# Performance work log

Hardware: AMD Instinct MI355X
Metric: run time of the kernel (lower is better)

The kernel has to match this reference:

```python
import jax, jax.numpy as jnp
import numpy as np
from jax.scipy.special import xlogy

LAMBDA_XM = 0.05
LAMBDA_SEG2D = 1.0
BN_EPS = 1e-5


def setup_inputs() -> dict:
    key = jax.random.key(0)
    ks = jax.random.split(key, 40)
    S, N, Nv, B, Np, M, H, C, MID = 2, 240000, 80000, 2, 120000, 30000, 64, 20, 16
    Nimg = B * M
    f = lambda i, shape, s=0.05: jax.random.normal(ks[i], shape, jnp.float32) * s
    inp = {
        'img_feat': f(0, (S, Nimg, H), 1.0),
        'pts_feat': f(1, (S, Nv, H), 1.0),
        'coors_inv': jax.random.randint(ks[2], (S, N), 0, Nv),
        'labels': jax.random.randint(ks[3], (N,), 0, C),
        'img_label': jax.random.randint(ks[4], (Nimg,), 0, C),
        'p2img_idx': jax.random.randint(ks[5], (B, M), 0, Np),
        # multihead 3d classifiers (per scale): Linear(H,128)-ReLU-Linear(128,C)
        'w3a': f(6, (S, H, 128)), 'b3a': jnp.zeros((S, 128)),
        'w3b': f(7, (S, 128, C)), 'b3b': jnp.zeros((S, C)),
        # multihead fuse classifiers
        'wfa': f(8, (S, H, 128)), 'bfa': jnp.zeros((S, 128)),
        'wfb': f(9, (S, 128, C)), 'bfb': jnp.zeros((S, C)),
        # attention: fc1(H->H//4), fc2(H->H//4), fc3(H//2->2), conv1/conv2 (1x1 -> linear) + BN
        'fc1w': f(10, (S, H, MID)), 'fc1b': jnp.zeros((S, MID)),
        'fc2w': f(11, (S, H, MID)), 'fc2b': jnp.zeros((S, MID)),
        'fc3w': f(12, (S, 2 * MID, 2)), 'fc3b': jnp.zeros((S, 2)),
        'c1w': f(13, (S, H, H)), 'c1b': jnp.zeros((S, H)),
        'bn1g': jnp.ones((S, H)), 'bn1b': jnp.zeros((S, H)),
        'c2w': f(14, (S, H, H)), 'c2b': jnp.zeros((S, H)),
        'bn2g': jnp.ones((S, H)), 'bn2b': jnp.zeros((S, H)),
        # final classifier Linear(S*H,128)-ReLU-Linear(128,C)
        'clw1': f(15, (S * H, 128)), 'clb1': jnp.zeros((128,)),
        'clw2': f(16, (128, C)), 'clb2': jnp.zeros((C,)),
    }
    return inp


def _mlp2(x, w1, b1, w2, b2):
    return jax.nn.relu(x @ w1 + b1) @ w2 + b2


def _ce(logits, lab):
    logp = jax.nn.log_softmax(logits, -1)
    return -jnp.take_along_axis(logp, lab[:, None], axis=1).mean()


def _lovasz(probs, lab):
    # lovasz-softmax over all classes, averaged over present classes
    C = probs.shape[1]
    fg = jax.nn.one_hot(lab, C, dtype=probs.dtype)  # [N,C]
    errors = jnp.abs(fg - probs)

    def per_class(err_c, fg_c):
        order = jnp.argsort(-err_c)
        e = err_c[order]
        f = fg_c[order]
        gts = f.sum()
        inter = gts - jnp.cumsum(f)
        union = gts + jnp.cumsum(1.0 - f)
        jac = 1.0 - inter / union
        jac = jnp.concatenate([jac[:1], jac[1:] - jac[:-1]])
        return jnp.dot(e, jac)

    losses = jax.vmap(per_class)(errors.T, fg.T)  # [C]
    present = (fg.sum(0) > 0).astype(probs.dtype)
    return jnp.sum(losses * present) / jnp.maximum(present.sum(), 1.0)


def _seg_loss(logits, lab):
    return _ce(logits, lab) + _lovasz(jax.nn.softmax(logits, -1), lab)


def _convbn_relu(x, cw, cb, g, b):
    # 1x1 Conv1d == per-point linear; BN (training-mode batch stats over points)
    y = x @ cw + cb
    mu = y.mean(0)
    var = y.var(0)
    return jax.nn.relu((y - mu) * jax.lax.rsqrt(var + BN_EPS) * g + b)


def reference(img_feat, pts_feat, coors_inv, labels, img_label, p2img_idx,
              w3a, b3a, w3b, b3b, wfa, bfa, wfb, bfb,
              fc1w, fc1b, fc2w, fc2b, fc3w, fc3b,
              c1w, c1b, bn1g, bn1b, c2w, c2b, bn2g, bn2b,
              clw1, clb1, clw2, clb2):
    S, Nv, H = pts_feat.shape
    C = w3b.shape[-1]
    B, M = p2img_idx.shape
    N = labels.shape[0]
    Np = N // B
    # p2img_mapping: per-batch gather composed to one global gather (batch blocks are contiguous/equal)
    gidx = (jnp.arange(B)[:, None] * Np + p2img_idx).reshape(-1)  # [Nimg]

    loss = jnp.float32(0.0)
    feats = []
    for s in range(S):
        pred3d = _mlp2(pts_feat[s], w3a[s], b3a[s], w3b[s], b3b[s])  # [Nv,C]
        # voxelize_labels: majority vote per voxel (== unique+scatter_max count argmax)
        counts = jnp.zeros((Nv, C), jnp.float32).at[coors_inv[s], labels].add(1.0)
        vox_lab = jnp.argmax(counts, axis=1)  # [Nv]
        # gather voxel feats/preds to image-projected points (fused gather)
        idx = coors_inv[s][gidx]  # [Nimg]
        p = pts_feat[s][idx]      # [Nimg,H] pseudo feats
        pts_pred = pred3d[idx]    # [Nimg,C]
        v = img_feat[s]           # [Nimg,H] valid (image) feats
        # Attention fusion
        w = jax.nn.sigmoid(
            jnp.concatenate([p @ fc1w[s] + fc1b[s], v @ fc2w[s] + fc2b[s]], -1) @ fc3w[s] + fc3b[s])  # [Nimg,2]
        fuse = (_convbn_relu(p, c1w[s], c1b[s], bn1g[s], bn1b[s]) * w[:, 0:1]
                + _convbn_relu(v, c2w[s], c2b[s], bn2g[s], bn2b[s]) * w[:, 1:2])
        feats.append(fuse)
        fuse_pred = _mlp2(fuse, wfa[s], bfa[s], wfb[s], bfb[s])
        loss = loss + _seg_loss(pred3d, vox_lab)
        loss = loss + _seg_loss(fuse_pred, img_label) * LAMBDA_SEG2D / S
        # F.kl_div(log_softmax(pts_pred), softmax(fuse_pred)), reduction='mean' over all elements
        pf = jax.nn.softmax(fuse_pred, -1)
        kl = jnp.mean(xlogy(pf, pf) - pf * jax.nn.log_softmax(pts_pred, -1))
        loss = loss + kl * LAMBDA_XM / S
    img_logits = _mlp2(jnp.concatenate(feats, -1), clw1, clb1, clw2, clb2)
    loss = loss + _seg_loss(img_logits, img_label)
    return loss
```

## Files before the change

kernel.cpp:

```cpp
#include <hip/hip_runtime.h>
#include <stdint.h>

static constexpr int NV   = 80000;
static constexpr int NPT  = 240000;
static constexpr int NIMG = 60000;
static constexpr int Hh   = 64;
static constexpr int Cc   = 20;
static constexpr int NPp  = 120000;
static constexpr int Mm   = 30000;
static constexpr int NB     = 8192;
static constexpr int NCH    = 16;
static constexpr int NBLK_GA  = (NIMG + 63) / 64;
static constexpr int NBLK_MLP = NV / 64;
static constexpr int NBLK_CNT = (NPT + 255) / 256;
static constexpr int NBLK_FILL_NV = (NV + 255) / 256;
static constexpr int NBLK_HIST = Cc * NCH;
static constexpr int NBLK_IDX  = (NIMG + 255) / 256;
#define BN_EPS 1e-5f

using bf16x8 = __attribute__((ext_vector_type(8))) short;
using f32x4  = __attribute__((ext_vector_type(4))) float;

__device__ __forceinline__ float waveReduce(float v) {
  #pragma unroll
  for (int o = 32; o > 0; o >>= 1) v += __shfl_down(v, o);
  return v;
}
__device__ __forceinline__ short f2bf(float f) {
  uint32_t u = __float_as_uint(f);
  return (short)((u + 0x7FFFu + ((u >> 16) & 1u)) >> 16);
}
__device__ __forceinline__ float bf2f(uint32_t h) { return __uint_as_float(h << 16); }
__device__ __forceinline__ uint32_t pk2(float a, float b) {
  return ((uint32_t)(uint16_t)f2bf(a)) | ((uint32_t)(uint16_t)f2bf(b) << 16);
}

struct PackDesc { const float* src; short* dst; int K, Nr, nt; };
struct PackArgs { PackDesc d[14]; };

__global__ void __launch_bounds__(256)
k_pack_zero(PackArgs pa,
            const float* __restrict__ fc1w, const float* __restrict__ fc1b,
            const float* __restrict__ fc2w, const float* __restrict__ fc2b,
            const float* __restrict__ fc3w, const float* __restrict__ fc3b,
            float* __restrict__ attEffs,
            uint4* __restrict__ zb, int zq,
            const int* __restrict__ ci0, const int* __restrict__ ci1,
            const int* __restrict__ p2img,
            int* __restrict__ idx0, int* __restrict__ idx1) {
  int bid = blockIdx.x;
  if (bid >= 384) {
    bid -= 384;
    if (bid < NBLK_IDX) {
      int i = bid * 256 + threadIdx.x;
      if (i < NIMG) idx0[i] = ci0[(i >= Mm ? NPp : 0) + p2img[i]];
    } else {
      int i = (bid - NBLK_IDX) * 256 + threadIdx.x;
      if (i < NIMG) idx1[i] = ci1[(i >= Mm ? NPp : 0) + p2img[i]];
    }
    return;
  }
  if (bid >= 128) {
    const uint4 z = make_uint4(0u, 0u, 0u, 0u);
    int i = (bid - 128) * 256 + threadIdx.x;
    for (; i < zq; i += 256 * 256) zb[i] = z;
    return;
  }
  const int stride = 128 * 256;
  for (int di = 0; di < 14; di++) {
    const float* src = pa.d[di].src;
    short* dst = pa.d[di].dst;
    int K = pa.d[di].K, Nr = pa.d[di].Nr, ntiles = pa.d[di].nt;
    int total = (K / 32) * ntiles * 512;
    for (int idx = bid * 256 + threadIdx.x; idx < total; idx += stride) {
      int j = idx & 7, lane = (idx >> 3) & 63, tile = idx >> 9;
      int nt = tile % ntiles, kt = tile / ntiles;
      int k = kt * 32 + (lane >> 4) * 8 + j;
      int n = nt * 16 + (lane & 15);
      float v = (n < Nr) ? src[(size_t)k * Nr + n] : 0.f;
      dst[idx] = f2bf(v);
    }
  }
  if (bid < 2 && threadIdx.x < 64) {
    int s = bid, t = threadIdx.x;
    const float* f1w = fc1w + s * 64 * 16; const float* f1b = fc1b + s * 16;
    const float* f2w = fc2w + s * 64 * 16; const float* f2b = fc2b + s * 16;
    const float* f3w = fc3w + s * 64;      const float* f3b = fc3b + s * 2;
    float* aE = attEffs + s * 320;
    float p0 = 0.f, p1 = 0.f, v0 = 0.f, v1 = 0.f;
    #pragma unroll
    for (int j = 0; j < 16; j++) {
      p0 = fmaf(f1w[t * 16 + j], f3w[j * 2], p0);
      p1 = fmaf(f1w[t * 16 + j], f3w[j * 2 + 1], p1);
      v0 = fmaf(f2w[t * 16 + j], f3w[(16 + j) * 2], v0);
      v1 = fmaf(f2w[t * 16 + j], f3w[(16 + j) * 2 + 1], v1);
    }
    aE[t * 2] = p0; aE[t * 2 + 1] = p1;
    aE[128 + t * 2] = v0; aE[128 + t * 2 + 1] = v1;
    if (t == 0) {
      float b0 = f3b[0], b1 = f3b[1];
      for (int j = 0; j < 16; j++) {
        b0 += f1b[j] * f3w[j * 2] + f2b[j] * f3w[(16 + j) * 2];
        b1 += f1b[j] * f3w[j * 2 + 1] + f2b[j] * f3w[(16 + j) * 2 + 1];
      }
      aE[256] = b0; aE[257] = b1;
    }
  }
}

__device__ void scanbin_body(const unsigned long long* __restrict__ H64,
                             int n, int call, float* __restrict__ lossesC5,
                             int* __restrict__ gts5, int cls) {
  __shared__ int sWC[4], sWF[4];
  __shared__ float sRedF[4];
  int t = threadIdx.x;
  int lane = t & 63, w = t >> 6;
  const uint4* Hv = (const uint4*)(H64 + (size_t)cls * NB + (size_t)t * 32);
  int locC = 0, locF = 0;
  #pragma unroll
  for (int i = 0; i < 16; i++) {
    uint4 u = Hv[i];
    locF += (int)(u.x + u.z);
    locC += (int)(u.y + u.w);
  }
  int sc = locC, sf = locF;
  #pragma unroll
  for (int o = 1; o < 64; o <<= 1) {
    int a = __shfl_up(sc, o);
    int b = __shfl_up(sf, o);
    if (lane >= o) { sc += a; sf += b; }
  }
  if (lane == 63) { sWC[w] = sc; sWF[w] = sf; }
  __syncthreads();
  int offC = 0, offF = 0, Ftot = 0;
  #pragma unroll
  for (int ww = 0; ww < 4; ww++) {
    int fc = sWF[ww];
    Ftot += fc;
    if (ww < w) { offC += sWC[ww]; offF += fc; }
  }
  int runC = offC + sc - locC;
  int runF = offF + sf - locF;
  float gts = (float)Ftot;
  float contrib = 0.f;
  #pragma unroll
  for (int i = 0; i < 16; i++) {
    uint4 u = Hv[i];
    #pragma unroll
    for (int j = 0; j < 2; j++) {
      int cnt = (int)(j ? u.w : u.y), fgc = (int)(j ? u.z : u.x);
      runC += cnt; runF += fgc;
      if (cnt > 0 && Ftot > 0) {
        float r0 = (float)(n - runC);
        float F0 = (float)(Ftot - runF);
        float r1 = r0 + (float)cnt;
        float F1 = F0 + (float)fgc;
        float emean = __uint_as_float((uint32_t)(t * 32 + i * 2 + j) << 17);
        contrib += emean * (r1 / (gts + r1 - F1) - r0 / (gts + r0 - F0));
      }
    }
  }
  contrib = waveReduce(contrib);
  if (lane == 0) sRedF[w] = contrib;
  __syncthreads();
  if (t == 0) {
    lossesC5[call * 32 + cls] = (Ftot > 0) ? (sRedF[0] + sRedF[1] + sRedF[2] + sRedF[3]) : 0.f;
    gts5[call * 32 + cls] = Ftot;
  }
}

__device__ void tile_loss(const float* __restrict__ sL, int r0, int rows, int n,
                          const int* __restrict__ lab, uint16_t* __restrict__ E,
                          float ceScale, float* __restrict__ lossAcc,
                          const float* __restrict__ pred3d, const int* __restrict__ idxg,
                          float klScale) {
  int t = threadIdx.x;
  if (t < 64) {
    float total = 0.f;
    int gr = r0 + t;
    if (gr < rows) {
      const float* l = sL + t * 21;
      float m = l[0];
      #pragma unroll
      for (int c = 1; c < Cc; c++) m = fmaxf(m, l[c]);
      float ex[Cc]; float se = 0.f;
      #pragma unroll
      for (int c = 0; c < Cc; c++) { ex[c] = expf(l[c] - m); se += ex[c]; }
      float inv = 1.f / se;
      float lse = logf(se);
      int lb = lab[gr];
      total = -(l[lb] - m - lse) * ceScale;
      #pragma unroll
      for (int c = 0; c < Cc; c++) {
        float prob = ex[c] * inv;
        int fg = (c == lb) ? 1 : 0;
        float err = fg ? (1.f - prob) : prob;
        err = fmaxf(err, 0.f);
        uint32_t key = __float_as_uint(err) >> 17;
        E[(size_t)c * n + gr] = (uint16_t)((key << 1) | (uint32_t)fg);
      }
      if (pred3d) {
        const float* q = pred3d + (size_t)idxg[gr] * Cc;
        float mq = q[0];
        #pragma unroll
        for (int c = 1; c < Cc; c++) mq = fmaxf(mq, q[c]);
        float sq = 0.f;
        #pragma unroll
        for (int c = 0; c < Cc; c++) sq += expf(q[c] - mq);
        float lsq = logf(sq);
        float kl = 0.f;
        #pragma unroll
        for (int c = 0; c < Cc; c++) {
          float lf = l[c] - m - lse;
          float pf = ex[c] * inv;
          float lq = q[c] - mq - lsq;
          kl += pf * (lf - lq);
        }
        total += kl * klScale;
      }
    }
    total = waveReduce(total);
    if (t == 0) atomicAdd(lossAcc, total);
  }
}

template<int D, bool TO_LDS>
__device__ __forceinline__ void mfma_mlp_core(const short* sXb, short* sH, float* sL,
    int r0, int rows,
    const short* __restrict__ pw1, const float* __restrict__ B1,
    const short* __restrict__ pw2, const float* __restrict__ B2,
    float* __restrict__ Out) {
  constexpr int LDB = D + 8;
  constexpr int KT1 = D / 32;
  const int t = threadIdx.x;
  const int lane = t & 63, w = t >> 6;
  const int m = lane & 15, quad = lane >> 4;
  const int rowA = 16 * w + m;
  bf16x8 a1[KT1];
  #pragma unroll
  for (int kt = 0; kt < KT1; kt++)
    a1[kt] = *(const bf16x8*)(sXb + rowA * LDB + kt * 32 + quad * 8);
  const bf16x8* b1 = (const bf16x8*)pw1;
  #pragma unroll
  for (int nt = 0; nt < 8; nt++) {
    f32x4 c = {0.f, 0.f, 0.f, 0.f};
    #pragma unroll
    for (int kt = 0; kt < KT1; kt++)
      c = __builtin_amdgcn_mfma_f32_16x16x32_bf16(a1[kt], b1[(kt * 8 + nt) * 64 + lane], c, 0, 0, 0);
    int col = nt * 16 + m;
    float bc = B1[col];
    #pragma unroll
    for (int reg = 0; reg < 4; reg++)
      sH[(16 * w + quad * 4 + reg) * 136 + col] = f2bf(fmaxf(c[reg] + bc, 0.f));
  }
  __syncthreads();
  bf16x8 a2[4];
  #pragma unroll
  for (int kt = 0; kt < 4; kt++)
    a2[kt] = *(const bf16x8*)(sH + rowA * 136 + kt * 32 + quad * 8);
  const bf16x8* b2 = (const bf16x8*)pw2;
  #pragma unroll
  for (int nt = 0; nt < 2; nt++) {
    f32x4 c = {0.f, 0.f, 0.f, 0.f};
    #pragma unroll
    for (int kt = 0; kt < 4; kt++)
      c = __builtin_amdgcn_mfma_f32_16x16x32_bf16(a2[kt], b2[(kt * 2 + nt) * 64 + lane], c, 0, 0, 0);
    int col = nt * 16 + m;
    if (col < Cc) {
      float bc = B2[col];
      #pragma unroll
      for (int reg = 0; reg < 4; reg++) {
        int rr = 16 * w + quad * 4 + reg;
        if (TO_LDS) {
          sL[rr * 21 + col] = c[reg] + bc;
        } else {
          int gr = r0 + rr;
          if (gr < rows) Out[(size_t)gr * Cc + col] = c[reg] + bc;
        }
      }
    }
  }
}

__device__ void mlp64_body(int bid0, const float* __restrict__ X,
    const short* __restrict__ pw1, const float* __restrict__ B1,
    const short* __restrict__ pw2, const float* __restrict__ B2,
    float* __restrict__ Out, int rows, char* smem) {
  short* sXb = (short*)smem;
  short* sH  = (short*)(smem + 9216);
  int t = threadIdx.x, r0 = bid0 * 64;
  for (int i = t; i < 1024; i += 256) {
    int r = i >> 4, k4 = (i & 15) * 4;
    int gr = r0 + r;
    float4 v = (gr < rows) ? *(const float4*)(X + (size_t)gr * 64 + k4)
                           : make_float4(0.f, 0.f, 0.f, 0.f);
    uint2 p; p.x = pk2(v.x, v.y); p.y = pk2(v.z, v.w);
    *(uint2*)(sXb + r * 72 + k4) = p;
  }
  __syncthreads();
  mfma_mlp_core<64, false>(sXb, sH, nullptr, r0, rows, pw1, B1, pw2, B2, Out);
}

__device__ void mlp128_loss_body(int bid0, const uint16_t* __restrict__ Xh,
    const short* __restrict__ pw1, const float* __restrict__ B1,
    const short* __restrict__ pw2, const float* __restrict__ B2,
    const int* __restrict__ lab, uint16_t* __restrict__ E, float ce,
    float* __restrict__ lossAcc, char* smem) {
  short* sXb = (short*)smem;
  short* sH  = (short*)(smem + 17408);
  int t = threadIdx.x, r0 = bid0 * 64;
  for (int i = t; i < 2048; i += 256) {
    int r = i >> 5, k4 = (i & 31) * 4;
    int gr = r0 + r;
    uint2 p = (gr < NIMG) ? *(const uint2*)(Xh + (size_t)gr * 128 + k4) : make_uint2(0u, 0u);
    *(uint2*)(sXb + r * 136 + k4) = p;
  }
  __syncthreads();
  mfma_mlp_core<128, true>(sXb, sH, (float*)sXb, r0, NIMG, pw1, B1, pw2, B2, nullptr);
  __syncthreads();
  tile_loss((float*)sXb, r0, NIMG, NIMG, lab, E, ce, lossAcc, nullptr, nullptr, 0.f);
}

__device__ void cnt_body(int bid0, const int* __restrict__ ci, const int* __restrict__ labels,
                         int* __restrict__ counts) {
  int i = bid0 * 256 + threadIdx.x;
  if (i < NPT) atomicAdd(&counts[(size_t)ci[i] * Cc + labels[i]], 1);
}

__device__ void colred_body(int bid0, const float* __restrict__ partials,
                            float* __restrict__ red64) {
  int t = threadIdx.x, j = bid0;
  float v = 0.f;
  for (int b = j; b < NBLK_GA; b += 64) v += partials[(size_t)b * 256 + t];
  red64[j * 256 + t] = v;
}

__device__ void fill_body(int bid0, const float* __restrict__ logits,
                          const int* __restrict__ vcnt,
                          int n, uint16_t* __restrict__ E,
                          float ceScale, float* __restrict__ lossAcc) {
  int i = bid0 * 256 + threadIdx.x;
  float total = 0.f;
  if (i < n) {
    const int* crow = vcnt + (size_t)i * Cc;
    int best = crow[0], lb = 0;
    #pragma unroll
    for (int k = 1; k < Cc; k++) {
      int ck = crow[k];
      if (ck > best) { best = ck; lb = k; }
    }
    const float* l = logits + (size_t)i * Cc;
    float m = l[0];
    #pragma unroll
    for (int c = 1; c < Cc; c++) m = fmaxf(m, l[c]);
    float ex[Cc]; float se = 0.f;
    #pragma unroll
    for (int c = 0; c < Cc; c++) { ex[c] = expf(l[c] - m); se += ex[c]; }
    float inv = 1.f / se;
    float lse = logf(se);
    total = -(l[lb] - m - lse) * ceScale;
    #pragma unroll
    for (int c = 0; c < Cc; c++) {
      float prob = ex[c] * inv;
      int fg = (c == lb) ? 1 : 0;
      float err = fg ? (1.f - prob) : prob;
      err = fmaxf(err, 0.f);
      uint32_t key = __float_as_uint(err) >> 17;
      E[(size_t)c * n + i] = (uint16_t)((key << 1) | (uint32_t)fg);
    }
  }
  total = waveReduce(total);
  __shared__ float sh[4];
  int lane = threadIdx.x & 63, w = threadIdx.x >> 6;
  if (lane == 0) sh[w] = total;
  __syncthreads();
  if (threadIdx.x == 0) atomicAdd(lossAcc, sh[0] + sh[1] + sh[2] + sh[3]);
}

__device__ void hist_body(int bid0, const uint16_t* __restrict__ E, int n,
                          unsigned long long* __restrict__ H64, char* smem) {
  uint32_t* lcf = (uint32_t*)smem;
  int t = threadIdx.x;
  int cls = bid0 / NCH, ch = bid0 - cls * NCH;
  int CHsz = (n + NCH - 1) / NCH;
  int i0 = ch * CHsz;
  int i1 = min(n, i0 + CHsz);
  for (int b = t; b < NB; b += 256) lcf[b] = 0u;
  __syncthreads();
  const uint16_t* Ec = E + (size_t)cls * n;
  for (int i = i0 + t; i < i1; i += 256) {
    uint32_t p = Ec[i];
    atomicAdd(&lcf[p >> 1], 0x10000u | (p & 1u));
  }
  __syncthreads();
  unsigned long long* Hc = H64 + (size_t)cls * NB;
  for (int b = t; b < NB; b += 256) {
    uint32_t v = lcf[b];
    if (v)
      atomicAdd(&Hc[b], ((unsigned long long)(v >> 16) << 32) | (v & 0xFFFFu));
  }
}

__device__ void gatt_body(int bid0, const float* __restrict__ pts, const int* __restrict__ idx,
                          const float* __restrict__ img,
                          const short* __restrict__ pc1, const float* __restrict__ c1b,
                          const short* __restrict__ pc2, const float* __restrict__ c2b,
                          const float* __restrict__ attEff,
                          uint16_t* __restrict__ y1, uint16_t* __restrict__ y2,
                          float* __restrict__ attw, float* __restrict__ partials,
                          char* smem) {
  short* sP = (short*)smem;
  short* sV = (short*)(smem + 9216);
  float* sAtt  = (float*)(smem + 18432);
  float* sStat = (float*)(smem + 20480);
  int t = threadIdx.x;
  int r0 = bid0 * 64;
  for (int i = t; i < 1024; i += 256) {
    int r = i >> 4, q = i & 15;
    int gr = r0 + r;
    float4 vp = make_float4(0.f, 0.f, 0.f, 0.f), vv = vp;
    if (gr < NIMG) {
      vp = *(const float4*)(pts + (size_t)idx[gr] * 64 + q * 4);
      vv = *(const float4*)(img + (size_t)gr * 64 + q * 4);
    }
    uint2 pp, qv;
    pp.x = pk2(vp.x, vp.y); pp.y = pk2(vp.z, vp.w);
    qv.x = pk2(vv.x, vv.y); qv.y = pk2(vv.z, vv.w);
    *(uint2*)(sP + r * 72 + q * 4) = pp;
    *(uint2*)(sV + r * 72 + q * 4) = qv;
  }
  __syncthreads();
  {
    int r = t & 63, qq = t >> 6;
    const float* aP = attEff;
    const float* aV = attEff + 128;
    float l0 = 0.f, l1 = 0.f;
    for (int k = qq * 16; k < qq * 16 + 16; k += 4) {
      uint2 up = *(const uint2*)(sP + r * 72 + k);
      uint2 uv = *(const uint2*)(sV + r * 72 + k);
      float p0 = bf2f(up.x & 0xffff), p1 = bf2f(up.x >> 16);
      float p2 = bf2f(up.y & 0xffff), p3 = bf2f(up.y >> 16);
      float v0 = bf2f(uv.x & 0xffff), v1 = bf2f(uv.x >> 16);
      float v2 = bf2f(uv.y & 0xffff), v3 = bf2f(uv.y >> 16);
      float4 wa = *(const float4*)(aP + 2 * k);
      float4 wb = *(const float4*)(aP + 2 * k + 4);
      l0 += p0 * wa.x + p1 * wa.z + p2 * wb.x + p3 * wb.z;
      l1 += p0 * wa.y + p1 * wa.w + p2 * wb.y + p3 * wb.w;
      float4 ua = *(const float4*)(aV + 2 * k);
      float4 ub = *(const float4*)(aV + 2 * k + 4);
      l0 += v0 * ua.x + v1 * ua.z + v2 * ub.x + v3 * ub.z;
      l1 += v0 * ua.y + v1 * ua.w + v2 * ub.y + v3 * ub.w;
    }
    sAtt[r * 8 + qq * 2] = l0;
    sAtt[r * 8 + qq * 2 + 1] = l1;
  }
  const int lane = t & 63, w = t >> 6;
  const int m = lane & 15, quad = lane >> 4;
  const int rowA = 16 * w + m;
  bf16x8 ap[2], av[2];
  #pragma unroll
  for (int kt = 0; kt < 2; kt++) {
    ap[kt] = *(const bf16x8*)(sP + rowA * 72 + kt * 32 + quad * 8);
    av[kt] = *(const bf16x8*)(sV + rowA * 72 + kt * 32 + quad * 8);
  }
  const bf16x8* b1 = (const bf16x8*)pc1;
  const bf16x8* b2 = (const bf16x8*)pc2;
  #pragma unroll
  for (int nt = 0; nt < 4; nt++) {
    int col = nt * 16 + m;
    f32x4 c1 = {0.f, 0.f, 0.f, 0.f}, c2 = {0.f, 0.f, 0.f, 0.f};
    #pragma unroll
    for (int kt = 0; kt < 2; kt++) {
      c1 = __builtin_amdgcn_mfma_f32_16x16x32_bf16(ap[kt], b1[(kt * 4 + nt) * 64 + lane], c1, 0, 0, 0);
      c2 = __builtin_amdgcn_mfma_f32_16x16x32_bf16(av[kt], b2[(kt * 4 + nt) * 64 + lane], c2, 0, 0, 0);
    }
    float bb1 = c1b[col], bb2 = c2b[col];
    float s1 = 0.f, q1 = 0.f, s2 = 0.f, q2 = 0.f;
    #pragma unroll
    for (int reg = 0; reg < 4; reg++) {
      int gr = r0 + 16 * w + quad * 4 + reg;
      if (gr < NIMG) {
        float v1 = c1[reg] + bb1, v2 = c2[reg] + bb2;
        y1[(size_t)gr * 64 + col] = (uint16_t)f2bf(v1);
        y2[(size_t)gr * 64 + col] = (uint16_t)f2bf(v2);
        s1 += v1; q1 = fmaf(v1, v1, q1);
        s2 += v2; q2 = fmaf(v2, v2, q2);
      }
    }
    s1 += __shfl_down(s1, 32); s1 += __shfl_down(s1, 16);
    q1 += __shfl_down(q1, 32); q1 += __shfl_down(q1, 16);
    s2 += __shfl_down(s2, 32); s2 += __shfl_down(s2, 16);
    q2 += __shfl_down(q2, 32); q2 += __shfl_down(q2, 16);
    if (lane < 16) {
      float* base = sStat + (w * 4 + nt) * 64 + lane;
      base[0]  = s1;
      base[16] = q1;
      base[32] = s2;
      base[48] = q2;
    }
  }
  __syncthreads();
  {
    int kind = t >> 6, col = t & 63;
    int nt = col >> 4, mm = col & 15;
    float v = 0.f;
    #pragma unroll
    for (int ww = 0; ww < 4; ww++)
      v += sStat[(ww * 4 + nt) * 64 + kind * 16 + mm];
    partials[(size_t)bid0 * 256 + kind * 64 + col] = v;
  }
  if (t < 64) {
    int gr = r0 + t;
    if (gr < NIMG) {
      float l0 = attEff[256] + sAtt[t * 8] + sAtt[t * 8 + 2] + sAtt[t * 8 + 4] + sAtt[t * 8 + 6];
      float l1 = attEff[257] + sAtt[t * 8 + 1] + sAtt[t * 8 + 3] + sAtt[t * 8 + 5] + sAtt[t * 8 + 7];
      attw[gr * 2]     = 1.f / (1.f + expf(-l0));
      attw[gr * 2 + 1] = 1.f / (1.f + expf(-l1));
    }
  }
}

__device__ void fusemlp_body(int bid0,
    const uint16_t* __restrict__ y1, const uint16_t* __restrict__ y2,
    const float* __restrict__ attw, const float* __restrict__ red64,
    const float* __restrict__ g1, const float* __restrict__ be1,
    const float* __restrict__ g2, const float* __restrict__ be2,
    uint16_t* __restrict__ feats, int s64,
    const short* __restrict__ pw1, const float* __restrict__ B1,
    const short* __restrict__ pw2, const float* __restrict__ B2,
    const int* __restrict__ lab, uint16_t* __restrict__ E, float ce,
    const float* __restrict__ pred3d, const int* __restrict__ idxg, float klScale,
    float* __restrict__ lossAcc, char* smem) {
  short* sXb = (short*)smem;
  short* sH  = (short*)(smem + 9216);
  float* sBn = (float*)(smem + 9216 + 17408);
  int t = threadIdx.x, r0 = bid0 * 64;
  float acc = 0.f;
  #pragma unroll 8
  for (int b = 0; b < 64; b++) acc += red64[b * 256 + t];
  float* sSum = (float*)sH;
  sSum[t] = acc;
  __syncthreads();
  if (t < 64) {
    float nn = (float)NIMG;
    float mu1 = sSum[t] / nn;
    float var1 = sSum[64 + t] / nn - mu1 * mu1;
    float a1 = g1[t] / sqrtf(var1 + BN_EPS);
    sBn[t] = a1; sBn[64 + t] = be1[t] - mu1 * a1;
    float mu2 = sSum[128 + t] / nn;
    float var2 = sSum[192 + t] / nn - mu2 * mu2;
    float a2 = g2[t] / sqrtf(var2 + BN_EPS);
    sBn[128 + t] = a2; sBn[192 + t] = be2[t] - mu2 * a2;
  }
  __syncthreads();
  for (int i = t; i < 1024; i += 256) {
    int r = i >> 4, q = i & 15;
    int gr = r0 + r;
    uint2 zp = make_uint2(0u, 0u);
    if (gr < NIMG) {
      float4 a1 = *(const float4*)(sBn + q * 4);
      float4 c1 = *(const float4*)(sBn + 64 + q * 4);
      float4 a2 = *(const float4*)(sBn + 128 + q * 4);
      float4 c2 = *(const float4*)(sBn + 192 + q * 4);
      uint2 u1 = *(const uint2*)(y1 + (size_t)gr * 64 + q * 4);
      uint2 u2 = *(const uint2*)(y2 + (size_t)gr * 64 + q * 4);
      float w0 = attw[gr * 2], w1 = attw[gr * 2 + 1];
      float zx = fmaxf(fmaf(bf2f(u1.x & 0xffff), a1.x, c1.x), 0.f) * w0
               + fmaxf(fmaf(bf2f(u2.x & 0xffff), a2.x, c2.x), 0.f) * w1;
      float zy = fmaxf(fmaf(bf2f(u1.x >> 16),   a1.y, c1.y), 0.f) * w0
               + fmaxf(fmaf(bf2f(u2.x >> 16),   a2.y, c2.y), 0.f) * w1;
      float zz = fmaxf(fmaf(bf2f(u1.y & 0xffff), a1.z, c1.z), 0.f) * w0
               + fmaxf(fmaf(bf2f(u2.y & 0xffff), a2.z, c2.z), 0.f) * w1;
      float zw = fmaxf(fmaf(bf2f(u1.y >> 16),   a1.w, c1.w), 0.f) * w0
               + fmaxf(fmaf(bf2f(u2.y >> 16),   a2.w, c2.w), 0.f) * w1;
      zp.x = pk2(zx, zy); zp.y = pk2(zz, zw);
      *(uint2*)(feats + (size_t)gr * 128 + s64 + q * 4) = zp;
    }
    *(uint2*)(sXb + r * 72 + q * 4) = zp;
  }
  __syncthreads();
  mfma_mlp_core<64, true>(sXb, sH, (float*)sXb, r0, NIMG, pw1, B1, pw2, B2, nullptr);
  __syncthreads();
  tile_loss((float*)sXb, r0, NIMG, NIMG, lab, E, ce, lossAcc, pred3d, idxg, klScale);
}

__global__ void __launch_bounds__(256)
k_mega2(const float* __restrict__ pf0, const float* __restrict__ pf1,
        const int* __restrict__ idx0, const int* __restrict__ idx1,
        const float* __restrict__ if0, const float* __restrict__ if1,
        const short* pc1w0, const short* pc1w1, const short* pc2w0, const short* pc2w1,
        const float* c1b, const float* c2b, const float* attEffs,
        uint16_t* y1a, uint16_t* y2a, uint16_t* y1b, uint16_t* y2b,
        float* attw0, float* attw1, float* partials0, float* partials1,
        const short* pw3a0, const float* b3a, const short* pw3b0, const float* b3b,
        const short* pw3a1, const short* pw3b1,
        float* pred3d0, float* pred3d1,
        const int* __restrict__ ci0, const int* __restrict__ ci1,
        const int* __restrict__ labels,
        int* __restrict__ counts0, int* __restrict__ counts1) {
  __shared__ char smem[26624];
  int bid = blockIdx.x;
  if (bid < NBLK_GA) {
    gatt_body(bid, pf0, idx0, if0, pc1w0, c1b, pc2w0, c2b, attEffs,
              y1a, y2a, attw0, partials0, smem);
    return;
  }
  bid -= NBLK_GA;
  if (bid < NBLK_GA) {
    gatt_body(bid, pf1, idx1, if1, pc1w1, c1b + 64, pc2w1, c2b + 64, attEffs + 320,
              y1b, y2b, attw1, partials1, smem);
    return;
  }
  bid -= NBLK_GA;
  if (bid < NBLK_MLP) { mlp64_body(bid, pf0, pw3a0, b3a, pw3b0, b3b, pred3d0, NV, smem); return; }
  bid -= NBLK_MLP;
  if (bid < NBLK_MLP) { mlp64_body(bid, pf1, pw3a1, b3a + 128, pw3b1, b3b + Cc, pred3d1, NV, smem); return; }
  bid -= NBLK_MLP;
  if (bid < NBLK_CNT) { cnt_body(bid, ci0, labels, counts0); return; }
  cnt_body(bid - NBLK_CNT, ci1, labels, counts1);
}

__global__ void __launch_bounds__(256)
k_fill_colred(const float* __restrict__ l0, const int* __restrict__ vc0, uint16_t* __restrict__ E0,
              const float* __restrict__ l1, const int* __restrict__ vc1, uint16_t* __restrict__ E1,
              float ce, float* __restrict__ lossAcc,
              const float* partials0, float* red64_0,
              const float* partials1, float* red64_1) {
  int bid = blockIdx.x;
  if (bid < NBLK_FILL_NV) {
    fill_body(bid, l0, vc0, NV, E0, ce, lossAcc);
    return;
  }
  bid -= NBLK_FILL_NV;
  if (bid < NBLK_FILL_NV) {
    fill_body(bid, l1, vc1, NV, E1, ce, lossAcc);
    return;
  }
  bid -= NBLK_FILL_NV;
  if (bid < 64) { colred_body(bid, partials0, red64_0); return; }
  colred_body(bid - 64, partials1, red64_1);
}

__global__ void __launch_bounds__(256)
k_fuse2_hist2(const uint16_t* y1a, const uint16_t* y2a, const float* attw0, const float* red64_0,
              const uint16_t* y1b, const uint16_t* y2b, const float* attw1, const float* red64_1,
              const float* bn1g, const float* bn1b, const float* bn2g, const float* bn2b,
              uint16_t* feats,
              const short* pwfa0, const float* bfa, const short* pwfb0, const float* bfb,
              const short* pwfa1, const short* pwfb1,
              const int* __restrict__ img_label, float ce, float kl, float* lossAcc,
              const float* pred3d0, const int* idx0, uint16_t* E3,
              const float* pred3d1, const int* idx1, uint16_t* E4,
              const uint16_t* __restrict__ E0, unsigned long long* H0,
              const uint16_t* __restrict__ E1, unsigned long long* H2) {
  __shared__ char smem[32768];
  int bid = blockIdx.x;
  if (bid < NBLK_GA) {
    fusemlp_body(bid, y1a, y2a, attw0, red64_0, bn1g, bn1b, bn2g, bn2b, feats, 0,
                 pwfa0, bfa, pwfb0, bfb,
                 img_label, E3, ce, pred3d0, idx0, kl, lossAcc, smem);
    return;
  }
  bid -= NBLK_GA;
  if (bid < NBLK_GA) {
    fusemlp_body(bid, y1b, y2b, attw1, red64_1, bn1g + 64, bn1b + 64, bn2g + 64, bn2b + 64,
                 feats, 64, pwfa1, bfa + 128, pwfb1, bfb + Cc,
                 img_label, E4, ce, pred3d1, idx1, kl, lossAcc, smem);
    return;
  }
  bid -= NBLK_GA;
  if (bid < NBLK_HIST) { hist_body(bid, E0, NV, H0, smem); return; }
  hist_body(bid - NBLK_HIST, E1, NV, H2, smem);
}

__global__ void __launch_bounds__(256)
k_finx2(const uint16_t* __restrict__ feats,
        const short* pcl1, const float* clb1, const short* pcl2, const float* clb2,
        const int* __restrict__ img_label, uint16_t* E2, float ce, float* lossAcc,
        const uint16_t* __restrict__ E3, unsigned long long* H1,
        const uint16_t* __restrict__ E4, unsigned long long* H3,
        const unsigned long long* H0, const unsigned long long* H2,
        float* lossesC5, int* gts5) {
  __shared__ char smem[34816];
  int bid = blockIdx.x;
  if (bid < NBLK_GA) {
    mlp128_loss_body(bid, feats, pcl1, clb1, pcl2, clb2, img_label, E2, ce, lossAcc, smem);
    return;
  }
  bid -= NBLK_GA;
  if (bid < NBLK_HIST) { hist_body(bid, E3, NIMG, H1, smem); return; }
  bid -= NBLK_HIST;
  if (bid < NBLK_HIST) { hist_body(bid, E4, NIMG, H3, smem); return; }
  bid -= NBLK_HIST;
  if (bid < Cc) { scanbin_body(H0, NV, 0, lossesC5, gts5, bid); return; }
  scanbin_body(H2, NV, 2, lossesC5, gts5, bid - Cc);
}

__global__ void __launch_bounds__(256)
k_hist_scan2(const uint16_t* __restrict__ E2, unsigned long long* H4,
             const unsigned long long* H1, const unsigned long long* H3,
             float* lossesC5, int* gts5) {
  __shared__ char smem[32768];
  int bid = blockIdx.x;
  if (bid < NBLK_HIST) { hist_body(bid, E2, NIMG, H4, smem); return; }
  bid -= NBLK_HIST;
  if (bid < Cc) { scanbin_body(H1, NIMG, 1, lossesC5, gts5, bid); return; }
  scanbin_body(H3, NIMG, 3, lossesC5, gts5, bid - Cc);
}

__global__ void __launch_bounds__(256)
k_scanbin5(const unsigned long long* H64, int n, int call,
           float* lossesC5, int* gts5) {
  scanbin_body(H64, n, call, lossesC5, gts5, blockIdx.x);
}

__global__ void k_final(const float* __restrict__ lossAcc,
                        const float* __restrict__ lossesC5, const int* __restrict__ gts5,
                        float* __restrict__ out) {
  const float coefs[5] = {1.0f, 0.5f, 1.0f, 0.5f, 1.0f};
  float loss = lossAcc[0];
  for (int call = 0; call < 5; call++) {
    float s = 0.f; int np = 0;
    for (int c = 0; c < Cc; c++)
      if (gts5[call * 32 + c] > 0) { s += lossesC5[call * 32 + c]; np++; }
    loss += coefs[call] * s / (float)(np > 0 ? np : 1);
  }
  out[0] = loss;
}

extern "C" void kernel_launch(void* const* d_in, const int* in_sizes, int n_in,
                              void* d_out, int out_size, void* d_ws, size_t ws_size,
                              hipStream_t stream) {
  const float* img_feat = (const float*)d_in[0];
  const float* pts_feat = (const float*)d_in[1];
  const int* coors_inv  = (const int*)d_in[2];
  const int* labels     = (const int*)d_in[3];
  const int* img_label  = (const int*)d_in[4];
  const int* p2img      = (const int*)d_in[5];
  const float* w3a = (const float*)d_in[6];
  const float* b3a = (const float*)d_in[7];
  const float* w3b = (const float*)d_in[8];
  const float* b3b = (const float*)d_in[9];
  const float* wfa = (const float*)d_in[10];
  const float* bfa = (const float*)d_in[11];
  const float* wfb = (const float*)d_in[12];
  const float* bfb = (const float*)d_in[13];
  const float* fc1w = (const float*)d_in[14];
  const float* fc1b = (const float*)d_in[15];
  const float* fc2w = (const float*)d_in[16];
  const float* fc2b = (const float*)d_in[17];
  const float* fc3w = (const float*)d_in[18];
  const float* fc3b = (const float*)d_in[19];
  const float* c1w  = (const float*)d_in[20];
  const float* c1b  = (const float*)d_in[21];
  const float* bn1g = (const float*)d_in[22];
  const float* bn1b = (const float*)d_in[23];
  const float* c2w  = (const float*)d_in[24];
  const float* c2b  = (const float*)d_in[25];
  const float* bn2g = (const float*)d_in[26];
  const float* bn2b = (const float*)d_in[27];
  const float* clw1 = (const float*)d_in[28];
  const float* clb1 = (const float*)d_in[29];
  const float* clw2 = (const float*)d_in[30];
  const float* clb2 = (const float*)d_in[31];
  (void)in_sizes; (void)n_in; (void)out_size; (void)ws_size;

  char* ws = (char*)d_ws;
  size_t off = 0;
  auto alloc = [&](size_t bytes) { void* p = ws + off; off += (bytes + 255) & ~(size_t)255; return p; };
  uint16_t* feats = (uint16_t*)alloc((size_t)NIMG * 128 * 2);
  float* pred3d0 = (float*)alloc((size_t)NV * Cc * 4);
  float* pred3d1 = (float*)alloc((size_t)NV * Cc * 4);
  int* idx0 = (int*)alloc((size_t)NIMG * 4);
  int* idx1 = (int*)alloc((size_t)NIMG * 4);
  uint16_t* y1a = (uint16_t*)alloc((size_t)NIMG * Hh * 2);
  uint16_t* y2a = (uint16_t*)alloc((size_t)NIMG * Hh * 2);
  uint16_t* y1b = (uint16_t*)alloc((size_t)NIMG * Hh * 2);
  uint16_t* y2b = (uint16_t*)alloc((size_t)NIMG * Hh * 2);
  uint16_t* E0 = (uint16_t*)alloc((size_t)Cc * NV * 2);
  uint16_t* E1 = (uint16_t*)alloc((size_t)Cc * NV * 2);
  uint16_t* E2 = (uint16_t*)alloc((size_t)Cc * NIMG * 2);
  uint16_t* E3 = (uint16_t*)alloc((size_t)Cc * NIMG * 2);
  uint16_t* E4 = (uint16_t*)alloc((size_t)Cc * NIMG * 2);
  float* partials0 = (float*)alloc((size_t)NBLK_GA * 256 * 4);
  float* partials1 = (float*)alloc((size_t)NBLK_GA * 256 * 4);
  float* red64_0 = (float*)alloc(64 * 256 * 4);
  float* red64_1 = (float*)alloc(64 * 256 * 4);
  float* attw0 = (float*)alloc((size_t)NIMG * 2 * 4);
  float* attw1 = (float*)alloc((size_t)NIMG * 2 * 4);
  short* pwAll = (short*)alloc(86016 * 2);
  short* pw3a0 = pwAll,          * pw3a1 = pwAll + 8192;
  short* pwfa0 = pwAll + 16384,  * pwfa1 = pwAll + 24576;
  short* pw3b0 = pwAll + 32768,  * pw3b1 = pwAll + 36864;
  short* pwfb0 = pwAll + 40960,  * pwfb1 = pwAll + 45056;
  short* pcl1  = pwAll + 49152;
  short* pcl2  = pwAll + 65536;
  short* pc1w0 = pwAll + 69632,  * pc1w1 = pwAll + 73728;
  short* pc2w0 = pwAll + 77824,  * pc2w1 = pwAll + 81920;
  float* attEffs = (float*)alloc(2 * 320 * 4);
  size_t zsize = 1024 + (size_t)5 * Cc * NB * 8 + (size_t)2 * NV * Cc * 4;
  char* zbase = (char*)alloc(zsize);
  float* lossAcc  = (float*)zbase;
  float* lossesC5 = (float*)zbase + 32;
  int*   gts5     = (int*)((float*)zbase + 192);
  unsigned long long* Hbase = (unsigned long long*)(zbase + 1024);
  auto Hc = [&](int call) { return Hbase + (size_t)call * Cc * NB; };
  int* counts0 = (int*)(zbase + 1024 + (size_t)5 * Cc * NB * 8);
  int* counts1 = counts0 + (size_t)NV * Cc;
  int zq = (int)(zsize / 16);

  const float kl = 0.025f / ((float)NIMG * Cc);
  const float* pf0 = pts_feat;
  const float* pf1 = pts_feat + (size_t)NV * Hh;
  const float* if0 = img_feat;
  const float* if1 = img_feat + (size_t)NIMG * Hh;
  const int* ci0 = coors_inv;
  const int* ci1 = coors_inv + NPT;

  PackArgs pa;
  pa.d[0]  = {w3a,        pw3a0, 64, 128, 8};
  pa.d[1]  = {w3a + 8192, pw3a1, 64, 128, 8};
  pa.d[2]  = {wfa,        pwfa0, 64, 128, 8};
  pa.d[3]  = {wfa + 8192, pwfa1, 64, 128, 8};
  pa.d[4]  = {w3b,        pw3b0, 128, 20, 2};
  pa.d[5]  = {w3b + 2560, pw3b1, 128, 20, 2};
  pa.d[6]  = {wfb,        pwfb0, 128, 20, 2};
  pa.d[7]  = {wfb + 2560, pwfb1, 128, 20, 2};
  pa.d[8]  = {clw1,       pcl1, 128, 128, 8};
  pa.d[9]  = {clw2,       pcl2, 128, 20, 2};
  pa.d[10] = {c1w,        pc1w0, 64, 64, 4};
  pa.d[11] = {c1w + 4096, pc1w1, 64, 64, 4};
  pa.d[12] = {c2w,        pc2w0, 64, 64, 4};
  pa.d[13] = {c2w + 4096, pc2w1, 64, 64, 4};
  k_pack_zero<<<384 + 2 * NBLK_IDX, 256, 0, stream>>>(
      pa, fc1w, fc1b, fc2w, fc2b, fc3w, fc3b, attEffs,
      (uint4*)zbase, zq, ci0, ci1, p2img, idx0, idx1);

  k_mega2<<<2 * NBLK_GA + 2 * NBLK_MLP + 2 * NBLK_CNT, 256, 0, stream>>>(
      pf0, pf1, idx0, idx1, if0, if1,
      pc1w0, pc1w1, pc2w0, pc2w1, c1b, c2b, attEffs,
      y1a, y2a, y1b, y2b, attw0, attw1, partials0, partials1,
      pw3a0, b3a, pw3b0, b3b, pw3a1, pw3b1, pred3d0, pred3d1,
      ci0, ci1, labels, counts0, counts1);

  k_fill_colred<<<2 * NBLK_FILL_NV + 128, 256, 0, stream>>>(
      pred3d0, counts0, E0, pred3d1, counts1, E1, 1.0f / NV, lossAcc,
      partials0, red64_0, partials1, red64_1);

  k_fuse2_hist2<<<2 * NBLK_GA + 2 * NBLK_HIST, 256, 0, stream>>>(
      y1a, y2a, attw0, red64_0, y1b, y2b, attw1, red64_1,
      bn1g, bn1b, bn2g, bn2b, feats,
      pwfa0, bfa, pwfb0, bfb, pwfa1, pwfb1,
      img_label, 0.5f / NIMG, kl, lossAcc,
      pred3d0, idx0, E3, pred3d1, idx1, E4,
      E0, Hc(0), E1, Hc(2));

  k_finx2<<<NBLK_GA + 2 * NBLK_HIST + 2 * Cc, 256, 0, stream>>>(
      feats, pcl1, clb1, pcl2, clb2,
      img_label, E2, 1.0f / NIMG, lossAcc,
      E3, Hc(1), E4, Hc(3),
      Hc(0), Hc(2), lossesC5, gts5);

  k_hist_scan2<<<NBLK_HIST + 2 * Cc, 256, 0, stream>>>(
      E2, Hc(4), Hc(1), Hc(3), lossesC5, gts5);

  k_scanbin5<<<Cc, 256, 0, stream>>>(Hc(4), NIMG, 4, lossesC5, gts5);

  k_final<<<1, 1, 0, stream>>>(lossAcc, lossesC5, gts5, (float*)d_out);
}
```

Before: 355.9 us.

## Pre-gather point features and pred3d rows into contiguous buffers in earlier kernels

```diff
diff --git a/kernel.cpp b/kernel.cpp
--- a/kernel.cpp
+++ b/kernel.cpp
@@ -15,7 +15,8 @@
 static constexpr int NBLK_CNT = (NPT + 255) / 256;
 static constexpr int NBLK_FILL_NV = (NV + 255) / 256;
 static constexpr int NBLK_HIST = Cc * NCH;
-static constexpr int NBLK_IDX  = (NIMG + 255) / 256;
+static constexpr int NBLK_GATH = 2 * NIMG * 8 / 256;
+static constexpr int NBLK_P3G  = (2 * NIMG + 255) / 256;
 #define BN_EPS 1e-5f
 
 using bf16x8 = __attribute__((ext_vector_type(8))) short;
@@ -47,17 +48,25 @@
             uint4* __restrict__ zb, int zq,
             const int* __restrict__ ci0, const int* __restrict__ ci1,
             const int* __restrict__ p2img,
-            int* __restrict__ idx0, int* __restrict__ idx1) {
+            int* __restrict__ idx0, int* __restrict__ idx1,
+            const float* __restrict__ pts, uint16_t* __restrict__ pgath) {
   int bid = blockIdx.x;
   if (bid >= 384) {
-    bid -= 384;
-    if (bid < NBLK_IDX) {
-      int i = bid * 256 + threadIdx.x;
-      if (i < NIMG) idx0[i] = ci0[(i >= Mm ? NPp : 0) + p2img[i]];
-    } else {
-      int i = (bid - NBLK_IDX) * 256 + threadIdx.x;
-      if (i < NIMG) idx1[i] = ci1[(i >= Mm ? NPp : 0) + p2img[i]];
-    }
+    int g = (bid - 384) * 256 + threadIdx.x;
+    int row = g >> 3, q = g & 7;
+    int r = (row >= NIMG) ? row - NIMG : row;
+    int s1 = (row >= NIMG) ? 1 : 0;
+    const int* ci = s1 ? ci1 : ci0;
+    int b = (r >= Mm) ? 1 : 0;
+    int id = ci[b * NPp + p2img[r]];
+    if (q == 0) { if (s1) idx1[r] = id; else idx0[r] = id; }
+    const float* src = pts + (size_t)s1 * NV * 64 + (size_t)id * 64 + q * 8;
+    float4 a = *(const float4*)src;
+    float4 c = *(const float4*)(src + 4);
+    uint4 o;
+    o.x = pk2(a.x, a.y); o.y = pk2(a.z, a.w);
+    o.z = pk2(c.x, c.y); o.w = pk2(c.z, c.w);
+    *(uint4*)(pgath + (size_t)row * 64 + q * 8) = o;
     return;
   }
   if (bid >= 128) {
@@ -172,8 +181,7 @@
 __device__ void tile_loss(const float* __restrict__ sL, int r0, int rows, int n,
                           const int* __restrict__ lab, uint16_t* __restrict__ E,
                           float ceScale, float* __restrict__ lossAcc,
-                          const float* __restrict__ pred3d, const int* __restrict__ idxg,
-                          float klScale) {
+                          const float* __restrict__ p3g, float klScale) {
   int t = threadIdx.x;
   if (t < 64) {
     float total = 0.f;
@@ -199,8 +207,8 @@
         uint32_t key = __float_as_uint(err) >> 17;
         E[(size_t)c * n + gr] = (uint16_t)((key << 1) | (uint32_t)fg);
       }
-      if (pred3d) {
-        const float* q = pred3d + (size_t)idxg[gr] * Cc;
+      if (p3g) {
+        const float* q = p3g + (size_t)gr * Cc;
         float mq = q[0];
         #pragma unroll
         for (int c = 1; c < Cc; c++) mq = fmaxf(mq, q[c]);
@@ -318,7 +326,7 @@
   __syncthreads();
   mfma_mlp_core<128, true>(sXb, sH, (float*)sXb, r0, NIMG, pw1, B1, pw2, B2, nullptr);
   __syncthreads();
-  tile_loss((float*)sXb, r0, NIMG, NIMG, lab, E, ce, lossAcc, nullptr, nullptr, 0.f);
+  tile_loss((float*)sXb, r0, NIMG, NIMG, lab, E, ce, lossAcc, nullptr, 0.f);
 }
 
 __device__ void cnt_body(int bid0, const int* __restrict__ ci, const int* __restrict__ labels,
@@ -333,6 +341,24 @@
   float v = 0.f;
   for (int b = j; b < NBLK_GA; b += 64) v += partials[(size_t)b * 256 + t];
   red64[j * 256 + t] = v;
+}
+
+__device__ void p3gath_body(int bid0, const float* __restrict__ pred3d0,
+                            const float* __restrict__ pred3d1,
+                            const int* __restrict__ idx0, const int* __restrict__ idx1,
+                            float* __restrict__ p3g0, float* __restrict__ p3g1) {
+  int row = bid0 * 256 + threadIdx.x;
+  if (row >= 2 * NIMG) return;
+  int s1 = (row >= NIMG) ? 1 : 0;
+  int r = s1 ? row - NIMG : row;
+  const float* pred = s1 ? pred3d1 : pred3d0;
+  float* dst = (s1 ? p3g1 : p3g0) + (size_t)r * Cc;
+  const float* src = pred + (size_t)(s1 ? idx1[r] : idx0[r]) * Cc;
+  #pragma unroll
+  for (int c = 0; c < Cc; c += 2) {
+    uint2 v = *(const uint2*)(src + c);
+    *(uint2*)(dst + c) = v;
+  }
 }
 
 __device__ void fill_body(int bid0, const float* __restrict__ logits,
@@ -401,7 +427,7 @@
   }
 }
 
-__device__ void gatt_body(int bid0, const float* __restrict__ pts, const int* __restrict__ idx,
+__device__ void gatt_body(int bid0, const uint16_t* __restrict__ pg,
                           const float* __restrict__ img,
                           const short* __restrict__ pc1, const float* __restrict__ c1b,
                           const short* __restrict__ pc2, const float* __restrict__ c2b,
@@ -415,18 +441,20 @@
   float* sStat = (float*)(smem + 20480);
   int t = threadIdx.x;
   int r0 = bid0 * 64;
+  for (int i = t; i < 512; i += 256) {
+    int r = i >> 3, q = i & 7;
+    int gr = r0 + r;
+    uint4 pv = make_uint4(0u, 0u, 0u, 0u);
+    if (gr < NIMG) pv = *(const uint4*)(pg + (size_t)gr * 64 + q * 8);
+    *(uint4*)(sP + r * 72 + q * 8) = pv;
+  }
   for (int i = t; i < 1024; i += 256) {
     int r = i >> 4, q = i & 15;
     int gr = r0 + r;
-    float4 vp = make_float4(0.f, 0.f, 0.f, 0.f), vv = vp;
-    if (gr < NIMG) {
-      vp = *(const float4*)(pts + (size_t)idx[gr] * 64 + q * 4);
-      vv = *(const float4*)(img + (size_t)gr * 64 + q * 4);
-    }
-    uint2 pp, qv;
-    pp.x = pk2(vp.x, vp.y); pp.y = pk2(vp.z, vp.w);
+    float4 vv = make_float4(0.f, 0.f, 0.f, 0.f);
+    if (gr < NIMG) vv = *(const float4*)(img + (size_t)gr * 64 + q * 4);
+    uint2 qv;
     qv.x = pk2(vv.x, vv.y); qv.y = pk2(vv.z, vv.w);
-    *(uint2*)(sP + r * 72 + q * 4) = pp;
     *(uint2*)(sV + r * 72 + q * 4) = qv;
   }
   __syncthreads();
@@ -529,7 +557,7 @@
     const short* __restrict__ pw1, const float* __restrict__ B1,
     const short* __restrict__ pw2, const float* __restrict__ B2,
     const int* __restrict__ lab, uint16_t* __restrict__ E, float ce,
-    const float* __restrict__ pred3d, const int* __restrict__ idxg, float klScale,
+    const float* __restrict__ p3g, float klScale,
     float* __restrict__ lossAcc, char* smem) {
   short* sXb = (short*)smem;
   short* sH  = (short*)(smem + 9216);
@@ -581,12 +609,12 @@
   __syncthreads();
   mfma_mlp_core<64, true>(sXb, sH, (float*)sXb, r0, NIMG, pw1, B1, pw2, B2, nullptr);
   __syncthreads();
-  tile_loss((float*)sXb, r0, NIMG, NIMG, lab, E, ce, lossAcc, pred3d, idxg, klScale);
+  tile_loss((float*)sXb, r0, NIMG, NIMG, lab, E, ce, lossAcc, p3g, klScale);
 }
 
 __global__ void __launch_bounds__(256)
 k_mega2(const float* __restrict__ pf0, const float* __restrict__ pf1,
-        const int* __restrict__ idx0, const int* __restrict__ idx1,
+        const uint16_t* __restrict__ pg0, const uint16_t* __restrict__ pg1,
         const float* __restrict__ if0, const float* __restrict__ if1,
         const short* pc1w0, const short* pc1w1, const short* pc2w0, const short* pc2w1,
         const float* c1b, const float* c2b, const float* attEffs,
@@ -601,13 +629,13 @@
   __shared__ char smem[26624];
   int bid = blockIdx.x;
   if (bid < NBLK_GA) {
-    gatt_body(bid, pf0, idx0, if0, pc1w0, c1b, pc2w0, c2b, attEffs,
+    gatt_body(bid, pg0, if0, pc1w0, c1b, pc2w0, c2b, attEffs,
               y1a, y2a, attw0, partials0, smem);
     return;
   }
   bid -= NBLK_GA;
   if (bid < NBLK_GA) {
-    gatt_body(bid, pf1, idx1, if1, pc1w1, c1b + 64, pc2w1, c2b + 64, attEffs + 320,
+    gatt_body(bid, pg1, if1, pc1w1, c1b + 64, pc2w1, c2b + 64, attEffs + 320,
               y1b, y2b, attw1, partials1, smem);
     return;
   }
@@ -625,7 +653,9 @@
               const float* __restrict__ l1, const int* __restrict__ vc1, uint16_t* __restrict__ E1,
               float ce, float* __restrict__ lossAcc,
               const float* partials0, float* red64_0,
-              const float* partials1, float* red64_1) {
+              const float* partials1, float* red64_1,
+              const int* __restrict__ idx0, const int* __restrict__ idx1,
+              float* __restrict__ p3g0, float* __restrict__ p3g1) {
   int bid = blockIdx.x;
   if (bid < NBLK_FILL_NV) {
     fill_body(bid, l0, vc0, NV, E0, ce, lossAcc);
@@ -638,7 +668,9 @@
   }
   bid -= NBLK_FILL_NV;
   if (bid < 64) { colred_body(bid, partials0, red64_0); return; }
-  colred_body(bid - 64, partials1, red64_1);
+  bid -= 64;
+  if (bid < 64) { colred_body(bid, partials1, red64_1); return; }
+  p3gath_body(bid - 64, l0, l1, idx0, idx1, p3g0, p3g1);
 }
 
 __global__ void __launch_bounds__(256)
@@ -649,8 +681,8 @@
               const short* pwfa0, const float* bfa, const short* pwfb0, const float* bfb,
               const short* pwfa1, const short* pwfb1,
               const int* __restrict__ img_label, float ce, float kl, float* lossAcc,
-              const float* pred3d0, const int* idx0, uint16_t* E3,
-              const float* pred3d1, const int* idx1, uint16_t* E4,
+              const float* p3g0, uint16_t* E3,
+              const float* p3g1, uint16_t* E4,
               const uint16_t* __restrict__ E0, unsigned long long* H0,
               const uint16_t* __restrict__ E1, unsigned long long* H2) {
   __shared__ char smem[32768];
@@ -658,14 +690,14 @@
   if (bid < NBLK_GA) {
     fusemlp_body(bid, y1a, y2a, attw0, red64_0, bn1g, bn1b, bn2g, bn2b, feats, 0,
                  pwfa0, bfa, pwfb0, bfb,
-                 img_label, E3, ce, pred3d0, idx0, kl, lossAcc, smem);
+                 img_label, E3, ce, p3g0, kl, lossAcc, smem);
     return;
   }
   bid -= NBLK_GA;
   if (bid < NBLK_GA) {
     fusemlp_body(bid, y1b, y2b, attw1, red64_1, bn1g + 64, bn1b + 64, bn2g + 64, bn2b + 64,
                  feats, 64, pwfa1, bfa + 128, pwfb1, bfb + Cc,
-                 img_label, E4, ce, pred3d1, idx1, kl, lossAcc, smem);
+                 img_label, E4, ce, p3g1, kl, lossAcc, smem);
     return;
   }
   bid -= NBLK_GA;
@@ -769,8 +801,11 @@
   size_t off = 0;
   auto alloc = [&](size_t bytes) { void* p = ws + off; off += (bytes + 255) & ~(size_t)255; return p; };
   uint16_t* feats = (uint16_t*)alloc((size_t)NIMG * 128 * 2);
+  uint16_t* pgath = (uint16_t*)alloc((size_t)2 * NIMG * 64 * 2);
   float* pred3d0 = (float*)alloc((size_t)NV * Cc * 4);
   float* pred3d1 = (float*)alloc((size_t)NV * Cc * 4);
+  float* p3g0 = (float*)alloc((size_t)NIMG * Cc * 4);
+  float* p3g1 = (float*)alloc((size_t)NIMG * Cc * 4);
   int* idx0 = (int*)alloc((size_t)NIMG * 4);
   int* idx1 = (int*)alloc((size_t)NIMG * 4);
   uint16_t* y1a = (uint16_t*)alloc((size_t)NIMG * Hh * 2);
@@ -816,6 +851,8 @@
   const float* if1 = img_feat + (size_t)NIMG * Hh;
   const int* ci0 = coors_inv;
   const int* ci1 = coors_inv + NPT;
+  uint16_t* pg0 = pgath;
+  uint16_t* pg1 = pgath + (size_t)NIMG * 64;
 
   PackArgs pa;
   pa.d[0]  = {w3a,        pw3a0, 64, 128, 8};
@@ -832,27 +869,28 @@
   pa.d[11] = {c1w + 4096, pc1w1, 64, 64, 4};
   pa.d[12] = {c2w,        pc2w0, 64, 64, 4};
   pa.d[13] = {c2w + 4096, pc2w1, 64, 64, 4};
-  k_pack_zero<<<384 + 2 * NBLK_IDX, 256, 0, stream>>>(
+  k_pack_zero<<<384 + NBLK_GATH, 256, 0, stream>>>(
       pa, fc1w, fc1b, fc2w, fc2b, fc3w, fc3b, attEffs,
-      (uint4*)zbase, zq, ci0, ci1, p2img, idx0, idx1);
+      (uint4*)zbase, zq, ci0, ci1, p2img, idx0, idx1, pts_feat, pgath);
 
   k_mega2<<<2 * NBLK_GA + 2 * NBLK_MLP + 2 * NBLK_CNT, 256, 0, stream>>>(
-      pf0, pf1, idx0, idx1, if0, if1,
+      pf0, pf1, pg0, pg1, if0, if1,
       pc1w0, pc1w1, pc2w0, pc2w1, c1b, c2b, attEffs,
       y1a, y2a, y1b, y2b, attw0, attw1, partials0, partials1,
       pw3a0, b3a, pw3b0, b3b, pw3a1, pw3b1, pred3d0, pred3d1,
       ci0, ci1, labels, counts0, counts1);
 
-  k_fill_colred<<<2 * NBLK_FILL_NV + 128, 256, 0, stream>>>(
+  k_fill_colred<<<2 * NBLK_FILL_NV + 128 + NBLK_P3G, 256, 0, stream>>>(
       pred3d0, counts0, E0, pred3d1, counts1, E1, 1.0f / NV, lossAcc,
-      partials0, red64_0, partials1, red64_1);
+      partials0, red64_0, partials1, red64_1,
+      idx0, idx1, p3g0, p3g1);
 
   k_fuse2_hist2<<<2 * NBLK_GA + 2 * NBLK_HIST, 256, 0, stream>>>(
       y1a, y2a, attw0, red64_0, y1b, y2b, attw1, red64_1,
       bn1g, bn1b, bn2g, bn2b, feats,
       pwfa0, bfa, pwfb0, bfb, pwfa1, pwfb1,
       img_label, 0.5f / NIMG, kl, lossAcc,
-      pred3d0, idx0, E3, pred3d1, idx1, E4,
+      p3g0, E3, p3g1, E4,
       E0, Hc(0), E1, Hc(2));
 
   k_finx2<<<NBLK_GA + 2 * NBLK_HIST + 2 * Cc, 256, 0, stream>>>(
```

New measurement: 356.6 us. Within noise of the previous version (+0.2%).
